# Performance work log

Measured on AMD Instinct MI355X. Metric: run time of the kernel, lower is better.

Reference implementation:

```python
import jax, jax.numpy as jnp
import numpy as np

N_NODES = 10000
N_EDGES = 50000
UNITS = 64
NUM_GAUSSIANS = 50
MIN_D, MAX_D, GAMMA = 0.0, 30.0, 10.0


def setup_inputs() -> dict:
    key = jax.random.key(0)
    ks = jax.random.split(key, 8)
    node_features = jax.random.normal(ks[0], (N_NODES, UNITS), dtype=jnp.float32)
    edge_indices = jax.random.randint(ks[1], (2, N_EDGES), 0, N_NODES, dtype=jnp.int32)
    distances = jax.random.uniform(ks[2], (N_EDGES,), dtype=jnp.float32) * MAX_D
    # filter network params (Dense(units) -> Dense(units*units)), glorot-ish scales
    W1 = jax.random.normal(ks[3], (NUM_GAUSSIANS, UNITS), dtype=jnp.float32) * 0.13
    b1 = jnp.zeros((UNITS,), dtype=jnp.float32)
    W2 = jax.random.normal(ks[4], (UNITS, UNITS * UNITS), dtype=jnp.float32) * 0.02
    b2 = jnp.zeros((UNITS * UNITS,), dtype=jnp.float32)
    # transform Dense(units, use_bias=False)
    Wt = jax.random.normal(ks[5], (UNITS, UNITS), dtype=jnp.float32) * 0.125
    return {"node_features": node_features, "edge_indices": edge_indices,
            "distances": distances, "W1": W1, "b1": b1, "W2": W2, "b2": b2, "Wt": Wt}


def reference(node_features, edge_indices, distances, W1, b1, W2, b2, Wt):
    # Gaussian basis expansion: [E, G]
    centers = jnp.linspace(MIN_D, MAX_D, NUM_GAUSSIANS, dtype=jnp.float32)
    dist_feat = jnp.exp(-GAMMA * jnp.square(distances[:, None] - centers[None, :]))
    # filter-generating network -> per-edge [E, U, U] filters
    h = dist_feat @ W1 + b1
    filters = (h @ W2 + b2).reshape(-1, UNITS, UNITS)
    # gather source node feats, linear transform, per-edge matvec
    src = node_features[edge_indices[0]]            # [E, U]
    transformed = src @ Wt                          # [E, U]
    filtered = jnp.einsum('eij,ej->ei', filters, transformed)  # [E, U]
    # scatter-sum to destination nodes
    messages = jax.ops.segment_sum(filtered, edge_indices[1], num_segments=N_NODES)
    # shifted softplus: f(0) = 0
    return jax.nn.softplus(messages) - jnp.log(jnp.float32(2.0))
```

## Files before the change

### kernel.cpp

```cpp
#include <hip/hip_runtime.h>
#include <stdint.h>

#define UNITS 64
#define UU 4096
#define NG 50
#define NSLOT 51
#define GAMMA_C 10.0f
#define STEP_C (30.0f / 49.0f)
#define NWIN 4
#define NBKT 47

typedef __attribute__((ext_vector_type(8))) short bf16x8;
typedef __attribute__((ext_vector_type(4))) float f32x4;

__device__ __forceinline__ uint16_t f2bf(float x) {
  uint32_t u = __float_as_uint(x);
  u += 0x7fffu + ((u >> 16) & 1u);
  return (uint16_t)(u >> 16);
}
__device__ __forceinline__ uint32_t pk_bf16(float lo, float hi) {
  uint32_t r;
  asm("v_cvt_pk_bf16_f32 %0, %1, %2" : "=v"(r) : "v"(lo), "v"(hi));
  return r;
}
__device__ __forceinline__ int lo_of(float d) {
  int lo = (int)floorf(d * (1.0f / STEP_C)) - 1;
  return min(max(lo, 0), NG - NWIN);
}

__global__ void __launch_bounds__(256) k_hist(const float* __restrict__ dist,
                                              int* __restrict__ bins,
                                              int* __restrict__ eidx, int E, int ne) {
  __shared__ int hloc[NBKT];
  for (int i = threadIdx.x; i < NBKT; i += 256) hloc[i] = 0;
  __syncthreads();
  int tt = blockIdx.x * 256 + threadIdx.x;
  for (int e = tt; e < E; e += 64 * 256)
    atomicAdd(&hloc[lo_of(dist[e])], 1);
  __syncthreads();
  for (int i = threadIdx.x; i < NBKT; i += 256)
    if (hloc[i]) atomicAdd(&bins[i], hloc[i]);
  for (int i = tt; i < ne; i += 64 * 256) eidx[i] = -1;
}

__global__ void __launch_bounds__(256) k_at(
    const float* __restrict__ W1, const float* __restrict__ b1,
    const float* __restrict__ W2, const float* __restrict__ b2,
    const float* __restrict__ Wt, const float* __restrict__ dist,
    uint16_t* __restrict__ T5B, float* __restrict__ msg,
    const int* __restrict__ bins, int* __restrict__ rsv, int* __restrict__ eidx,
    int n_out, int E) {
  int g = blockIdx.y, bx = blockIdx.x;
  if (g >= NSLOT) {
    if (g < NSLOT + 8) {
      int n4 = n_out >> 2;
      float4 z = {0.f, 0.f, 0.f, 0.f};
      for (int t = ((g - NSLOT) * 16 + bx) * 256 + threadIdx.x; t < n4; t += 128 * 256)
        reinterpret_cast<float4*>(msg)[t] = z;
      return;
    }
    __shared__ int sbase[NBKT];
    __shared__ int hcnt[NBKT], hbase[NBKT], hcur[NBKT];
    int sb = (g - (NSLOT + 8)) * 16 + bx;
    int per = (E + 63) >> 6;
    int e0 = sb * per, e1 = min(e0 + per, E);
    if (threadIdx.x < 64) {
      int lane = threadIdx.x;
      int cap = (lane < NBKT) ? ((bins[lane] + 15) & ~15) : 0;
      int inc = cap;
      #pragma unroll
      for (int s = 1; s < 64; s <<= 1) {
        int t = __shfl_up(inc, s, 64);
        if (lane >= s) inc += t;
      }
      if (lane < NBKT) sbase[lane] = inc - cap;
    }
    for (int i = threadIdx.x; i < NBKT; i += 256) { hcnt[i] = 0; hcur[i] = 0; }
    __syncthreads();
    for (int e = e0 + threadIdx.x; e < e1; e += 256)
      atomicAdd(&hcnt[lo_of(dist[e])], 1);
    __syncthreads();
    for (int i = threadIdx.x; i < NBKT; i += 256)
      hbase[i] = hcnt[i] ? (sbase[i] + atomicAdd(&rsv[i], hcnt[i])) : 0;
    __syncthreads();
    for (int e = e0 + threadIdx.x; e < e1; e += 256) {
      int b = lo_of(dist[e]);
      int p = hbase[b] + atomicAdd(&hcur[b], 1);
      eidx[p] = e;
    }
    return;
  }
  __shared__ float Aloc[256];
  __shared__ float WtL[64 * 65];
  const int t = threadIdx.x;
  const int ij = bx * 256 + t;

  #pragma unroll
  for (int q = 0; q < 4; ++q) {
    int idx = q * 256 + t;
    float4 v = reinterpret_cast<const float4*>(Wt)[idx];
    int mm = idx >> 4, jj = (idx & 15) * 4;
    float* dst = &WtL[mm * 65 + jj];
    dst[0] = v.x; dst[1] = v.y; dst[2] = v.z; dst[3] = v.w;
  }
  {
    float acc = 0.f;
    if (g < NG) {
      const float* w1r = W1 + g * UNITS;
      #pragma unroll 8
      for (int k = 0; k < UNITS; ++k) acc = fmaf(w1r[k], W2[k * UU + ij], acc);
    } else {
      #pragma unroll 8
      for (int k = 0; k < UNITS; ++k) acc = fmaf(b1[k], W2[k * UU + ij], acc);
      acc += b2[ij];
    }
    Aloc[t] = acc;
  }
  __syncthreads();

  const int i_local = t >> 6, m = t & 63;
  const float* ar = &Aloc[i_local * 64];
  const float* wr = &WtL[m * 65];
  float acc = 0.f;
  #pragma unroll 8
  for (int j = 0; j < UNITS; ++j) acc = fmaf(ar[j], wr[j], acc);
  const int gi = bx * 4 + i_local;
  T5B[(((g << 3) + (m >> 3)) << 9) + (gi << 3) + (m & 7)] = f2bf(acc);
}

__global__ void __launch_bounds__(256) k_em(
    const float* __restrict__ nf, const int* __restrict__ ei,
    const float* __restrict__ dist, const uint16_t* __restrict__ T5B,
    const int* __restrict__ eidx, const int* __restrict__ bins,
    float* __restrict__ msg, int E) {
  __shared__ float tile[4][16 * 64];
  int w = threadIdx.x >> 6, l = threadIdx.x & 63;
  int lr = l & 15, lg = l >> 4;
  int tileW = blockIdx.x * 4 + w;

  int c = (l < NBKT) ? bins[l] : 0;
  int tcap = (c + 15) >> 4;
  int p = tcap;
  #pragma unroll
  for (int s = 1; s < 64; s <<= 1) {
    int tt = __shfl_up(p, s, 64);
    if (l >= s) p += tt;
  }
  int total = __shfl(p, 63);
  if (tileW >= total) return;

  uint64_t mb = __ballot(tileW < p);
  int b = __ffsll((unsigned long long)mb) - 1;
  int pb = __shfl(p, b), tb = __shfl(tcap, b);
  int lt = tileW - (pb - tb);

  int e = eidx[(pb - tb + lt) * 16 + lr];
  bool valid = (e >= 0);
  int src = valid ? ei[e] : 0;
  int dst = valid ? ei[E + e] : -1;
  float d = valid ? dist[e] : 3.0e30f;

  float df[5];
  #pragma unroll
  for (int s = 0; s < NWIN; ++s) {
    float tt = d - (float)(b + s) * STEP_C;
    df[s] = __expf(-GAMMA_C * tt * tt);
  }
  df[NWIN] = valid ? 1.f : 0.f;

  union { bf16x8 v; uint32_t u[4]; } afr[2];
  const float4* ab = reinterpret_cast<const float4*>(nf + src * UNITS) + lg * 2;
  #pragma unroll
  for (int kk = 0; kk < 2; ++kk) {
    float4 v0 = ab[kk * 8], v1 = ab[kk * 8 + 1];
    afr[kk].u[0] = pk_bf16(v0.x, v0.y);
    afr[kk].u[1] = pk_bf16(v0.z, v0.w);
    afr[kk].u[2] = pk_bf16(v1.x, v1.y);
    afr[kk].u[3] = pk_bf16(v1.z, v1.w);
  }

  f32x4 run[4] = {};
  #pragma unroll
  for (int s = 0; s < 5; ++s) {
    int g = (s < NWIN) ? (b + s) : NG;
    const char* bb = (const char*)T5B + (g << 13) + (lg << 10) + (lr << 6);
    f32x4 acc[4] = {};
    #pragma unroll
    for (int kk = 0; kk < 2; ++kk)
      #pragma unroll
      for (int nt = 0; nt < 4; ++nt) {
        bf16x8 bf = *reinterpret_cast<const bf16x8*>(bb + (kk << 12) + (nt << 4));
        acc[nt] = __builtin_amdgcn_mfma_f32_16x16x32_bf16(afr[kk].v, bf, acc[nt], 0, 0, 0);
      }
    float dfq[4];
    #pragma unroll
    for (int q = 0; q < 4; ++q) dfq[q] = __shfl(df[s], lg * 4 + q, 64);
    #pragma unroll
    for (int nt = 0; nt < 4; ++nt)
      #pragma unroll
      for (int q = 0; q < 4; ++q)
        run[nt][q] = fmaf(dfq[q], acc[nt][q], run[nt][q]);
  }

  float* tw = tile[w];
  #pragma unroll
  for (int q = 0; q < 4; ++q) {
    float4 v4 = {run[0][q], run[1][q], run[2][q], run[3][q]};
    *reinterpret_cast<float4*>(&tw[(lg * 4 + q) * 64 + 4 * lr]) = v4;
  }
  asm volatile("" ::: "memory");

  #pragma unroll
  for (int r = 0; r < 16; ++r) {
    int dr = __shfl(dst, r, 64);
    if (dr < 0) continue;
    atomicAdd(&msg[dr * UNITS + l], tw[r * 64 + l]);
  }
}

__global__ void k_final(const float* __restrict__ msg, float* __restrict__ out,
                        int n_out) {
  int i4 = blockIdx.x * 256 + threadIdx.x;
  if (i4 >= (n_out >> 2)) return;
  float4 a = reinterpret_cast<const float4*>(msg)[i4];
  float4 r;
  r.x = ((a.x > 0.f) ? (a.x + log1pf(__expf(-a.x))) : log1pf(__expf(a.x))) - 0.69314718056f;
  r.y = ((a.y > 0.f) ? (a.y + log1pf(__expf(-a.y))) : log1pf(__expf(a.y))) - 0.69314718056f;
  r.z = ((a.z > 0.f) ? (a.z + log1pf(__expf(-a.z))) : log1pf(__expf(a.z))) - 0.69314718056f;
  r.w = ((a.w > 0.f) ? (a.w + log1pf(__expf(-a.w))) : log1pf(__expf(a.w))) - 0.69314718056f;
  reinterpret_cast<float4*>(out)[i4] = r;
}

extern "C" void kernel_launch(void* const* d_in, const int* in_sizes, int n_in,
                              void* d_out, int out_size, void* d_ws, size_t ws_size,
                              hipStream_t stream) {
  const float* nf   = (const float*)d_in[0];
  const int*   ei   = (const int*)d_in[1];
  const float* dist = (const float*)d_in[2];
  const float* W1   = (const float*)d_in[3];
  const float* b1   = (const float*)d_in[4];
  const float* W2   = (const float*)d_in[5];
  const float* b2   = (const float*)d_in[6];
  const float* Wt   = (const float*)d_in[7];
  float* out = (float*)d_out;

  int E = in_sizes[2];
  int n_out = out_size;

  int mt = E / 16 + NBKT + 1;
  int ne = mt * 16;

  char* ws = (char*)d_ws;
  size_t off_msg  = 417792;
  size_t off_bins = off_msg + (size_t)n_out * 4;
  size_t off_rsv  = off_bins + 64 * 4;
  size_t off_eidx = off_rsv + 64 * 4;

  uint16_t* T5B  = (uint16_t*)ws;
  float*    msg  = (float*)(ws + off_msg);
  int*      bins = (int*)(ws + off_bins);
  int*      rsv  = (int*)(ws + off_rsv);
  int*      eidx = (int*)(ws + off_eidx);

  hipMemsetAsync(bins, 0, 128 * 4, stream);

  k_hist<<<64, 256, 0, stream>>>(dist, bins, eidx, E, ne);
  k_at  <<<dim3(16, NSLOT + 12), 256, 0, stream>>>(W1, b1, W2, b2, Wt, dist,
                                                   T5B, msg, bins, rsv, eidx, n_out, E);
  k_em  <<<(mt + 3) / 4, 256, 0, stream>>>(nf, ei, dist, T5B, eidx, bins, msg, E);
  k_final<<<((n_out >> 2) + 255) / 256, 256, 0, stream>>>(msg, out, n_out);
}
```

Measured before the change: 44.92 us.

## Use per-chunk histograms for deterministic bucketing and process two tiles per wave

The histogram kernel now writes per-chunk bucket counts instead of global atomics, so the memset and the second histogram pass in the scatter step go away. Each scatter block computes its bucket base offsets from prefix sums over the chunk histograms. The edge-message kernel now handles two 16-edge tiles per wave, with the gathers for both issued up front to overlap load latency and halve the grid. The cost is redundant reads of the 64x64 count table in every block and wave, plus higher register pressure in the message kernel.

```diff
diff --git a/kernel.cpp b/kernel.cpp
--- a/kernel.cpp
+++ b/kernel.cpp
@@ -9,9 +9,12 @@
 #define STEP_C (30.0f / 49.0f)
 #define NWIN 4
 #define NBKT 47
+#define NCHK 64
 
 typedef __attribute__((ext_vector_type(8))) short bf16x8;
 typedef __attribute__((ext_vector_type(4))) float f32x4;
+
+union bfr_t { bf16x8 v; uint32_t u[4]; };
 
 __device__ __forceinline__ uint16_t f2bf(float x) {
   uint32_t u = __float_as_uint(x);
@@ -29,18 +32,19 @@
 }
 
 __global__ void __launch_bounds__(256) k_hist(const float* __restrict__ dist,
-                                              int* __restrict__ bins,
+                                              int* __restrict__ binsB,
                                               int* __restrict__ eidx, int E, int ne) {
   __shared__ int hloc[NBKT];
   for (int i = threadIdx.x; i < NBKT; i += 256) hloc[i] = 0;
   __syncthreads();
-  int tt = blockIdx.x * 256 + threadIdx.x;
-  for (int e = tt; e < E; e += 64 * 256)
+  int per = (E + NCHK - 1) / NCHK;
+  int e0 = blockIdx.x * per, e1 = min(e0 + per, E);
+  for (int e = e0 + threadIdx.x; e < e1; e += 256)
     atomicAdd(&hloc[lo_of(dist[e])], 1);
   __syncthreads();
-  for (int i = threadIdx.x; i < NBKT; i += 256)
-    if (hloc[i]) atomicAdd(&bins[i], hloc[i]);
-  for (int i = tt; i < ne; i += 64 * 256) eidx[i] = -1;
+  for (int i = threadIdx.x; i < 64; i += 256)
+    binsB[blockIdx.x * 64 + i] = (i < NBKT) ? hloc[i] : 0;
+  for (int i = blockIdx.x * 256 + threadIdx.x; i < ne; i += NCHK * 256) eidx[i] = -1;
 }
 
 __global__ void __launch_bounds__(256) k_at(
@@ -48,7 +52,7 @@
     const float* __restrict__ W2, const float* __restrict__ b2,
     const float* __restrict__ Wt, const float* __restrict__ dist,
     uint16_t* __restrict__ T5B, float* __restrict__ msg,
-    const int* __restrict__ bins, int* __restrict__ rsv, int* __restrict__ eidx,
+    const int* __restrict__ binsB, int* __restrict__ eidx,
     int n_out, int E) {
   int g = blockIdx.y, bx = blockIdx.x;
   if (g >= NSLOT) {
@@ -59,29 +63,27 @@
         reinterpret_cast<float4*>(msg)[t] = z;
       return;
     }
-    __shared__ int sbase[NBKT];
-    __shared__ int hcnt[NBKT], hbase[NBKT], hcur[NBKT];
+    __shared__ int hbase[NBKT], hcur[NBKT];
     int sb = (g - (NSLOT + 8)) * 16 + bx;
-    int per = (E + 63) >> 6;
+    int per = (E + NCHK - 1) / NCHK;
     int e0 = sb * per, e1 = min(e0 + per, E);
     if (threadIdx.x < 64) {
       int lane = threadIdx.x;
-      int cap = (lane < NBKT) ? ((bins[lane] + 15) & ~15) : 0;
+      int tot = 0, pre = 0;
+      for (int j = 0; j < NCHK; ++j) {
+        int v = binsB[j * 64 + lane];
+        tot += v;
+        if (j < sb) pre += v;
+      }
+      int cap = (tot + 15) & ~15;
       int inc = cap;
       #pragma unroll
       for (int s = 1; s < 64; s <<= 1) {
         int t = __shfl_up(inc, s, 64);
         if (lane >= s) inc += t;
       }
-      if (lane < NBKT) sbase[lane] = inc - cap;
-    }
-    for (int i = threadIdx.x; i < NBKT; i += 256) { hcnt[i] = 0; hcur[i] = 0; }
-    __syncthreads();
-    for (int e = e0 + threadIdx.x; e < e1; e += 256)
-      atomicAdd(&hcnt[lo_of(dist[e])], 1);
-    __syncthreads();
-    for (int i = threadIdx.x; i < NBKT; i += 256)
-      hbase[i] = hcnt[i] ? (sbase[i] + atomicAdd(&rsv[i], hcnt[i])) : 0;
+      if (lane < NBKT) { hbase[lane] = (inc - cap) + pre; hcur[lane] = 0; }
+    }
     __syncthreads();
     for (int e = e0 + threadIdx.x; e < e1; e += 256) {
       int b = lo_of(dist[e]);
@@ -131,15 +133,16 @@
 __global__ void __launch_bounds__(256) k_em(
     const float* __restrict__ nf, const int* __restrict__ ei,
     const float* __restrict__ dist, const uint16_t* __restrict__ T5B,
-    const int* __restrict__ eidx, const int* __restrict__ bins,
+    const int* __restrict__ eidx, const int* __restrict__ binsB,
     float* __restrict__ msg, int E) {
   __shared__ float tile[4][16 * 64];
   int w = threadIdx.x >> 6, l = threadIdx.x & 63;
   int lr = l & 15, lg = l >> 4;
-  int tileW = blockIdx.x * 4 + w;
-
-  int c = (l < NBKT) ? bins[l] : 0;
-  int tcap = (c + 15) >> 4;
+
+  int tot = 0;
+  #pragma unroll 8
+  for (int j = 0; j < NCHK; ++j) tot += binsB[j * 64 + l];
+  int tcap = (tot + 15) >> 4;
   int p = tcap;
   #pragma unroll
   for (int s = 1; s < 64; s <<= 1) {
@@ -147,75 +150,92 @@
     if (l >= s) p += tt;
   }
   int total = __shfl(p, 63);
-  if (tileW >= total) return;
-
-  uint64_t mb = __ballot(tileW < p);
-  int b = __ffsll((unsigned long long)mb) - 1;
-  int pb = __shfl(p, b), tb = __shfl(tcap, b);
-  int lt = tileW - (pb - tb);
-
-  int e = eidx[(pb - tb + lt) * 16 + lr];
-  bool valid = (e >= 0);
-  int src = valid ? ei[e] : 0;
-  int dst = valid ? ei[E + e] : -1;
-  float d = valid ? dist[e] : 3.0e30f;
-
-  float df[5];
-  #pragma unroll
-  for (int s = 0; s < NWIN; ++s) {
-    float tt = d - (float)(b + s) * STEP_C;
-    df[s] = __expf(-GAMMA_C * tt * tt);
-  }
-  df[NWIN] = valid ? 1.f : 0.f;
-
-  union { bf16x8 v; uint32_t u[4]; } afr[2];
-  const float4* ab = reinterpret_cast<const float4*>(nf + src * UNITS) + lg * 2;
-  #pragma unroll
-  for (int kk = 0; kk < 2; ++kk) {
-    float4 v0 = ab[kk * 8], v1 = ab[kk * 8 + 1];
-    afr[kk].u[0] = pk_bf16(v0.x, v0.y);
-    afr[kk].u[1] = pk_bf16(v0.z, v0.w);
-    afr[kk].u[2] = pk_bf16(v1.x, v1.y);
-    afr[kk].u[3] = pk_bf16(v1.z, v1.w);
-  }
-
-  f32x4 run[4] = {};
-  #pragma unroll
-  for (int s = 0; s < 5; ++s) {
-    int g = (s < NWIN) ? (b + s) : NG;
-    const char* bb = (const char*)T5B + (g << 13) + (lg << 10) + (lr << 6);
-    f32x4 acc[4] = {};
-    #pragma unroll
-    for (int kk = 0; kk < 2; ++kk)
-      #pragma unroll
-      for (int nt = 0; nt < 4; ++nt) {
-        bf16x8 bf = *reinterpret_cast<const bf16x8*>(bb + (kk << 12) + (nt << 4));
-        acc[nt] = __builtin_amdgcn_mfma_f32_16x16x32_bf16(afr[kk].v, bf, acc[nt], 0, 0, 0);
-      }
-    float dfq[4];
-    #pragma unroll
-    for (int q = 0; q < 4; ++q) dfq[q] = __shfl(df[s], lg * 4 + q, 64);
-    #pragma unroll
-    for (int nt = 0; nt < 4; ++nt)
-      #pragma unroll
-      for (int q = 0; q < 4; ++q)
-        run[nt][q] = fmaf(dfq[q], acc[nt][q], run[nt][q]);
+
+  int tA = (blockIdx.x * 4 + w) * 2, tB = tA + 1;
+  if (tA >= total) return;
+  bool actB = (tB < total);
+
+  uint64_t mA = __ballot(tA < p);
+  int bA = __ffsll((unsigned long long)mA) - 1;
+  int bB = bA;
+  if (actB) {
+    uint64_t mB = __ballot(tB < p);
+    bB = __ffsll((unsigned long long)mB) - 1;
+  }
+
+  int eA = eidx[tA * 16 + lr];
+  int eB = actB ? eidx[tB * 16 + lr] : -1;
+  bool vA = (eA >= 0), vB = (eB >= 0);
+  int srcA = vA ? ei[eA] : 0, dstA = vA ? ei[E + eA] : -1;
+  int srcB = vB ? ei[eB] : 0, dstB = vB ? ei[E + eB] : -1;
+  float dA = vA ? dist[eA] : 3.0e30f;
+  float dB = vB ? dist[eB] : 3.0e30f;
+
+  bfr_t afrA[2], afrB[2];
+  {
+    const float4* abA = reinterpret_cast<const float4*>(nf + srcA * UNITS) + lg * 2;
+    const float4* abB = reinterpret_cast<const float4*>(nf + srcB * UNITS) + lg * 2;
+    #pragma unroll
+    for (int kk = 0; kk < 2; ++kk) {
+      float4 a0 = abA[kk * 8], a1 = abA[kk * 8 + 1];
+      float4 b0 = abB[kk * 8], b1 = abB[kk * 8 + 1];
+      afrA[kk].u[0] = pk_bf16(a0.x, a0.y); afrA[kk].u[1] = pk_bf16(a0.z, a0.w);
+      afrA[kk].u[2] = pk_bf16(a1.x, a1.y); afrA[kk].u[3] = pk_bf16(a1.z, a1.w);
+      afrB[kk].u[0] = pk_bf16(b0.x, b0.y); afrB[kk].u[1] = pk_bf16(b0.z, b0.w);
+      afrB[kk].u[2] = pk_bf16(b1.x, b1.y); afrB[kk].u[3] = pk_bf16(b1.z, b1.w);
+    }
   }
 
   float* tw = tile[w];
-  #pragma unroll
-  for (int q = 0; q < 4; ++q) {
-    float4 v4 = {run[0][q], run[1][q], run[2][q], run[3][q]};
-    *reinterpret_cast<float4*>(&tw[(lg * 4 + q) * 64 + 4 * lr]) = v4;
-  }
-  asm volatile("" ::: "memory");
-
-  #pragma unroll
-  for (int r = 0; r < 16; ++r) {
-    int dr = __shfl(dst, r, 64);
-    if (dr < 0) continue;
-    atomicAdd(&msg[dr * UNITS + l], tw[r * 64 + l]);
-  }
+  auto run_tile = [&](int b, float d, bool valid, int dst, bfr_t* afr) {
+    float df[5];
+    #pragma unroll
+    for (int s = 0; s < NWIN; ++s) {
+      float tt = d - (float)(b + s) * STEP_C;
+      df[s] = __expf(-GAMMA_C * tt * tt);
+    }
+    df[NWIN] = valid ? 1.f : 0.f;
+
+    f32x4 run[4] = {};
+    #pragma unroll
+    for (int s = 0; s < 5; ++s) {
+      int g = (s < NWIN) ? (b + s) : NG;
+      const char* bb = (const char*)T5B + (g << 13) + (lg << 10) + (lr << 6);
+      f32x4 acc[4] = {};
+      #pragma unroll
+      for (int kk = 0; kk < 2; ++kk)
+        #pragma unroll
+        for (int nt = 0; nt < 4; ++nt) {
+          bf16x8 bf = *reinterpret_cast<const bf16x8*>(bb + (kk << 12) + (nt << 4));
+          acc[nt] = __builtin_amdgcn_mfma_f32_16x16x32_bf16(afr[kk].v, bf, acc[nt], 0, 0, 0);
+        }
+      float dfq[4];
+      #pragma unroll
+      for (int q = 0; q < 4; ++q) dfq[q] = __shfl(df[s], lg * 4 + q, 64);
+      #pragma unroll
+      for (int nt = 0; nt < 4; ++nt)
+        #pragma unroll
+        for (int q = 0; q < 4; ++q)
+          run[nt][q] = fmaf(dfq[q], acc[nt][q], run[nt][q]);
+    }
+
+    #pragma unroll
+    for (int q = 0; q < 4; ++q) {
+      float4 v4 = {run[0][q], run[1][q], run[2][q], run[3][q]};
+      *reinterpret_cast<float4*>(&tw[(lg * 4 + q) * 64 + 4 * lr]) = v4;
+    }
+    asm volatile("" ::: "memory");
+
+    #pragma unroll
+    for (int r = 0; r < 16; ++r) {
+      int dr = __shfl(dst, r, 64);
+      if (dr < 0) continue;
+      atomicAdd(&msg[dr * UNITS + l], tw[r * 64 + l]);
+    }
+  };
+
+  run_tile(bA, dA, vA, dstA, afrA);
+  if (actB) run_tile(bB, dB, vB, dstB, afrB);
 }
 
 __global__ void k_final(const float* __restrict__ msg, float* __restrict__ out,
@@ -251,22 +271,18 @@
   int ne = mt * 16;
 
   char* ws = (char*)d_ws;
-  size_t off_msg  = 417792;
-  size_t off_bins = off_msg + (size_t)n_out * 4;
-  size_t off_rsv  = off_bins + 64 * 4;
-  size_t off_eidx = off_rsv + 64 * 4;
-
-  uint16_t* T5B  = (uint16_t*)ws;
-  float*    msg  = (float*)(ws + off_msg);
-  int*      bins = (int*)(ws + off_bins);
-  int*      rsv  = (int*)(ws + off_rsv);
-  int*      eidx = (int*)(ws + off_eidx);
-
-  hipMemsetAsync(bins, 0, 128 * 4, stream);
-
-  k_hist<<<64, 256, 0, stream>>>(dist, bins, eidx, E, ne);
+  size_t off_msg   = 417792;
+  size_t off_binsB = off_msg + (size_t)n_out * 4;
+  size_t off_eidx  = off_binsB + NCHK * 64 * 4;
+
+  uint16_t* T5B   = (uint16_t*)ws;
+  float*    msg   = (float*)(ws + off_msg);
+  int*      binsB = (int*)(ws + off_binsB);
+  int*      eidx  = (int*)(ws + off_eidx);
+
+  k_hist<<<NCHK, 256, 0, stream>>>(dist, binsB, eidx, E, ne);
   k_at  <<<dim3(16, NSLOT + 12), 256, 0, stream>>>(W1, b1, W2, b2, Wt, dist,
-                                                   T5B, msg, bins, rsv, eidx, n_out, E);
-  k_em  <<<(mt + 3) / 4, 256, 0, stream>>>(nf, ei, dist, T5B, eidx, bins, msg, E);
+                                                   T5B, msg, binsB, eidx, n_out, E);
+  k_em  <<<(mt + 7) / 8, 256, 0, stream>>>(nf, ei, dist, T5B, eidx, binsB, msg, E);
   k_final<<<((n_out >> 2) + 255) / 256, 256, 0, stream>>>(msg, out, n_out);
 }
```

Result: faster. 43.10 us, median of 2 (-4.1%).
